# Kernel optimization log

Measured on AMD Instinct MI355X. Metric: run time of the kernel, lower is better.

The kernel has to match this reference:

```python
import jax, jax.numpy as jnp
import numpy as np

LATENT, COND, HID, OUT = 256, 64, 1024, 128
BATCH, MAX_LEN = 256, 512


def setup_inputs() -> dict:
    key = jax.random.key(0)
    ks = jax.random.split(key, 16)
    s = lambda fan_in: 1.0 / np.sqrt(fan_in)
    inp = {
        "latent_vector": jax.random.normal(ks[0], (BATCH, LATENT), jnp.float32),
        "conditions": jax.random.normal(ks[1], (BATCH, COND), jnp.float32),
        "output_lengths": jax.random.randint(ks[2], (BATCH,), 0, MAX_LEN, jnp.int32),
        # latent_to_hidden / latent_to_cell / latent_to_start
        "W_h": jax.random.uniform(ks[3], (HID, LATENT), jnp.float32, -s(LATENT), s(LATENT)),
        "b_h": jax.random.uniform(ks[4], (HID,), jnp.float32, -s(LATENT), s(LATENT)),
        "W_c": jax.random.uniform(ks[5], (HID, LATENT), jnp.float32, -s(LATENT), s(LATENT)),
        "b_c": jax.random.uniform(ks[6], (HID,), jnp.float32, -s(LATENT), s(LATENT)),
        "W_s": jax.random.uniform(ks[7], (OUT, LATENT), jnp.float32, -s(LATENT), s(LATENT)),
        "b_s": jax.random.uniform(ks[8], (OUT,), jnp.float32, -s(LATENT), s(LATENT)),
        # LSTM (PyTorch layout: gates i,f,g,o stacked -> 4*HID rows)
        "W_ih": jax.random.uniform(ks[9], (4 * HID, OUT + COND), jnp.float32, -s(HID), s(HID)),
        "W_hh": jax.random.uniform(ks[10], (4 * HID, HID), jnp.float32, -s(HID), s(HID)),
        "b_ih": jax.random.uniform(ks[11], (4 * HID,), jnp.float32, -s(HID), s(HID)),
        "b_hh": jax.random.uniform(ks[12], (4 * HID,), jnp.float32, -s(HID), s(HID)),
        # hidden_to_output
        "W_out": jax.random.uniform(ks[13], (OUT, HID), jnp.float32, -s(HID), s(HID)),
        "b_out": jax.random.uniform(ks[14], (OUT,), jnp.float32, -s(HID), s(HID)),
    }
    return inp


def reference(latent_vector, conditions, output_lengths, W_h, b_h, W_c, b_c, W_s, b_s,
              W_ih, W_hh, b_ih, b_hh, W_out, b_out):
    h0 = latent_vector @ W_h.T + b_h            # [B, HID]
    c0 = latent_vector @ W_c.T + b_c            # [B, HID]
    x0 = latent_vector @ W_s.T + b_s            # [B, OUT]
    bias = b_ih + b_hh                          # fuse the two LSTM biases

    def step(carry, _):
        h, c, x = carry
        inp = jnp.concatenate([x, conditions], axis=-1)   # [B, OUT+COND]
        gates = inp @ W_ih.T + h @ W_hh.T + bias          # [B, 4*HID]
        i, f, g, o = jnp.split(gates, 4, axis=-1)
        i = jax.nn.sigmoid(i)
        f = jax.nn.sigmoid(f)
        g = jnp.tanh(g)
        o = jax.nn.sigmoid(o)
        c_new = f * c + i * g
        h_new = o * jnp.tanh(c_new)
        y = h_new @ W_out.T + b_out                        # [B, OUT]
        return (h_new, c_new, y), y

    _, ys = jax.lax.scan(step, (h0, c0, x0), None, length=MAX_LEN)  # [T, B, OUT]
    outputs = jnp.transpose(ys, (1, 0, 2))                           # [B, T, OUT]
    # mask positions >= output_lengths[i] to zero
    t = jnp.arange(MAX_LEN)                                          # [T]
    mask = (t[None, :] < output_lengths[:, None]).astype(outputs.dtype)  # [B, T]
    return outputs * mask[:, :, None]
```

## Files before the change

kernel.cpp:

```cpp
#include <hip/hip_runtime.h>

#define BB   256
#define LAT  256
#define CND  64
#define HID  1024
#define OUTD 128
#define TLEN 512
#define GIN  192
#define G4   4096

typedef _Float16 f16x8 __attribute__((ext_vector_type(8)));
typedef float    f32x4 __attribute__((ext_vector_type(4)));

#define MFMA16(A,B,C) __builtin_amdgcn_mfma_f32_16x16x32_f16((A),(B),(C),0,0,0)

__device__ __forceinline__ float fsig(float x) {
  return 1.0f / (1.0f + exp2f(-1.4426950408889634f * x));
}
__device__ __forceinline__ float ftanh_(float x) {
  return 2.0f / (1.0f + exp2f(2.8853900817779268f * (-x))) - 1.0f;
}

__device__ __forceinline__ f16x8 ldg_sc_h8(const void* p) {
  f16x8 v;
  asm volatile("global_load_dwordx4 %0, %1, off sc0 sc1" : "=v"(v) : "v"(p));
  return v;
}
__device__ __forceinline__ void stg_sc_h(void* p, _Float16 v) {
  unsigned u = (unsigned)__builtin_bit_cast(unsigned short, v);
  asm volatile("global_store_short %0, %1, off sc0 sc1" :: "v"(p), "v"(u) : "memory");
}
__device__ __forceinline__ void stg_sc_f32(void* p, float v) {
  asm volatile("global_store_dword %0, %1, off sc0 sc1" :: "v"(p), "v"(v) : "memory");
}

template<int N> __device__ __forceinline__ void waitvm() {
  if constexpr (N == 8) asm volatile("s_waitcnt vmcnt(8)" ::: "memory");
  else                  asm volatile("s_waitcnt vmcnt(0)" ::: "memory");
  __builtin_amdgcn_sched_barrier(0);
}
#define LDSBAR() { asm volatile("s_waitcnt lgkmcnt(0)" ::: "memory"); \
                   __builtin_amdgcn_s_barrier(); \
                   __builtin_amdgcn_sched_barrier(0); }


__global__ void prep_init(const float* __restrict__ lat,
                          const float* __restrict__ Wh, const float* __restrict__ bh,
                          const float* __restrict__ Wc, const float* __restrict__ bc,
                          const float* __restrict__ Ws, const float* __restrict__ bs,
                          float* __restrict__ h0, _Float16* __restrict__ hF,
                          float* __restrict__ c0, float* __restrict__ x0)
{
  __shared__ float lat_s[8][LAT];
  int tid = threadIdx.x;
  int b0 = blockIdx.y * 8;
  for (int bb = 0; bb < 8; ++bb)
    lat_s[bb][tid] = lat[(size_t)(b0 + bb) * LAT + tid];
  __syncthreads();
  int col = blockIdx.x * 256 + tid;
  if (col >= 2 * HID + OUTD) return;
  const float* wr; float bias; int kind; int cc;
  if (col < HID)            { cc = col;           wr = Wh + (size_t)cc * LAT; bias = bh[cc]; kind = 0; }
  else if (col < 2 * HID)   { cc = col - HID;     wr = Wc + (size_t)cc * LAT; bias = bc[cc]; kind = 1; }
  else                      { cc = col - 2 * HID; wr = Ws + (size_t)cc * LAT; bias = bs[cc]; kind = 2; }
  float acc[8];
#pragma unroll
  for (int bb = 0; bb < 8; ++bb) acc[bb] = bias;
  for (int k = 0; k < LAT; ++k) {
    float wv = wr[k];
#pragma unroll
    for (int bb = 0; bb < 8; ++bb) acc[bb] += lat_s[bb][k] * wv;
  }
  for (int bb = 0; bb < 8; ++bb) {
    int b = b0 + bb;
    if (kind == 0) {
      float v = acc[bb];
      h0[(size_t)b*HID + cc] = v;
      hF[(size_t)b*HID + cc] = (_Float16)v;
    }
    else if (kind == 1) { c0[(size_t)b*HID + cc] = acc[bb]; }
    else                { x0[(size_t)b*OUTD + cc] = acc[bb]; }
  }
}

__global__ void prep_d(const float* __restrict__ h0, const float* __restrict__ Wout,
                       const float* __restrict__ bout, const float* __restrict__ x0,
                       float* __restrict__ d)
{
  int t = blockIdx.x * 256 + threadIdx.x;
  int b = t >> 7, o = t & 127;
  const float* wr = Wout + (size_t)o * HID;
  const float* hr = h0 + (size_t)b * HID;
  float acc = bout[o];
  for (int k = 0; k < HID; ++k) acc += hr[k] * wr[k];
  d[t] = x0[t] - acc;
}

__global__ void prep_weff(const float* __restrict__ Whh, const float* __restrict__ Wih,
                          const float* __restrict__ Wout, _Float16* __restrict__ WeffH)
{
  int k = blockIdx.x * 256 + threadIdx.x;
  int n0 = blockIdx.y * 16;
  float acc[16];
#pragma unroll
  for (int nn = 0; nn < 16; ++nn) acc[nn] = Whh[(size_t)(n0 + nn) * HID + k];
  for (int j = 0; j < OUTD; ++j) {
    float wo = Wout[(size_t)j * HID + k];
#pragma unroll
    for (int nn = 0; nn < 16; ++nn) acc[nn] += Wih[(size_t)(n0 + nn) * GIN + j] * wo;
  }
#pragma unroll
  for (int nn = 0; nn < 16; ++nn)
    WeffH[(size_t)(n0 + nn) * HID + k] = (_Float16)acc[nn];
}

__global__ void prep_wob(const float* __restrict__ Wout, _Float16* __restrict__ Wob) {
  int t = blockIdx.x * 256 + threadIdx.x;
  Wob[t] = (_Float16)Wout[t];
}

__global__ void prep_bias(const float* __restrict__ cond, const float* __restrict__ Wih,
                          const float* __restrict__ bih, const float* __restrict__ bhh,
                          const float* __restrict__ bout, const float* __restrict__ d,
                          float* __restrict__ biasR, float* __restrict__ biasS)
{
  __shared__ float cond_s[8][CND];
  __shared__ float d_s[8][OUTD];
  int tid = threadIdx.x;
  int b0 = blockIdx.y * 8;
  for (int qq = 0; qq < 2; ++qq) {
    int idx = qq * 256 + tid;
    cond_s[idx >> 6][idx & 63] = cond[(size_t)(b0 + (idx >> 6)) * CND + (idx & 63)];
  }
  for (int qq = 0; qq < 4; ++qq) {
    int idx = qq * 256 + tid;
    d_s[idx >> 7][idx & 127] = d[(size_t)(b0 + (idx >> 7)) * OUTD + (idx & 127)];
  }
  __syncthreads();
  int n = blockIdx.x * 256 + tid;
  const float* wi = Wih + (size_t)n * GIN;
  float base = bih[n] + bhh[n];
  float aR[8], aS[8];
#pragma unroll
  for (int bb = 0; bb < 8; ++bb) { aR[bb] = 0.f; aS[bb] = 0.f; }
  for (int c = 0; c < CND; ++c) {
    float wv = wi[OUTD + c];
#pragma unroll
    for (int bb = 0; bb < 8; ++bb) aR[bb] += cond_s[bb][c] * wv;
  }
  for (int o = 0; o < OUTD; ++o) {
    float wv = wi[o];
    float bo = bout[o];
#pragma unroll
    for (int bb = 0; bb < 8; ++bb) { aR[bb] += bo * wv; aS[bb] += d_s[bb][o] * wv; }
  }
  for (int bb = 0; bb < 8; ++bb) {
    size_t idx = (size_t)(b0 + bb) * G4 + n;
    biasR[idx] = base + aR[bb];
    biasS[idx] = base + aR[bb] + aS[bb];
  }
}


__global__ __launch_bounds__(256, 1)
void lstm_main(_Float16* hF, const float* __restrict__ c0g,
               const float* __restrict__ biasR, const float* __restrict__ biasS,
               const _Float16* __restrict__ WeffH, const _Float16* __restrict__ Wob,
               const float* __restrict__ bout, const int* __restrict__ len,
               float* __restrict__ out, unsigned* bar)
{
  __shared__ __align__(16) char lds[67584];
  const int wg = blockIdx.x;
  const int xcd = wg & 7, slot = wg >> 3;
  const int q = slot >> 2, mt = slot & 3;
  const int nt = q * 8 + xcd;
  const int tid = threadIdx.x;
  const int w = tid >> 6, lane = tid & 63;
  const int l15 = lane & 15, lh = lane >> 4;
  const int rowA = w * 16 + l15;
  const int bD0 = mt * 64 + w * 16 + lh * 4;
  const int j = nt * 16 + l15;
  const bool doy = (nt < 8);
  const int oy = doy ? nt * 16 + l15 : 0;
  const float bo = doy ? bout[oy] : 0.0f;

  const char* wb[4];
#pragma unroll
  for (int g = 0; g < 4; ++g)
    wb[g] = (const char*)(WeffH + ((size_t)(g * HID + nt * 16 + l15)) * HID + lh * 8);
  const char* wbY = (const char*)(Wob + (size_t)oy * HID + lh * 8);

  float c[4]; int mylen[4]; float biasRv[16];
#pragma unroll
  for (int r = 0; r < 4; ++r) {
    c[r] = c0g[(size_t)(bD0 + r) * HID + j];
    mylen[r] = len[bD0 + r];
    size_t bi = (size_t)(bD0 + r) * G4 + nt * 16 + l15;
#pragma unroll
    for (int g = 0; g < 4; ++g) biasRv[r * 4 + g] = biasR[bi + (size_t)g * HID];
  }

  const _Float16* cb0[8];
  int rc8[8];
#pragma unroll
  for (int i = 0; i < 8; ++i) {
    int s = i * 256 + tid;
    int r = s >> 5, cc = s & 31;
    cb0[i] = hF + ((size_t)(mt * 64 + r) * HID + cc * 8);
    rc8[i] = r * 528 + cc * 16;
  }
  const int rdoff = rowA * 528 + lh * 16;
  _Float16* hb0[4];
#pragma unroll
  for (int r = 0; r < 4; ++r) hb0[r] = hF + ((size_t)(bD0 + r) * HID + j);

  unsigned* const myarr = bar + (size_t)(mt * 8 + xcd) * 64;

  f32x4 accM[4], accyM;
  f16x8 pfb[2][8];

  for (int t = 0; t < TLEN; ++t) {
    const size_t parin  = (size_t)(t & 1) * (BB * HID);
    const size_t parout = (size_t)((t + 1) & 1) * (BB * HID);

    auto issue = [&](int K) {
#pragma unroll
      for (int i = 0; i < 8; ++i)
        pfb[K & 1][i] = ldg_sc_h8(cb0[i] + parin + K * 256);
    };
    auto dswr = [&](int K) {
      char* Bb = lds + (K & 1) * 33792;
#pragma unroll
      for (int i = 0; i < 8; ++i)
        *(f16x8*)(Bb + rc8[i]) = pfb[K & 1][i];
    };
    auto comp = [&](int K) {
      const char* Bb = lds + (K & 1) * 33792;
#pragma unroll
      for (int kc = 0; kc < 8; ++kc) {
        f16x8 aH = *(const f16x8*)(Bb + rdoff + kc * 64);
        const int wo = K * 512 + kc * 64;
#pragma unroll
        for (int g = 0; g < 4; ++g) {
          f16x8 wH = *(const f16x8*)(wb[g] + wo);
          accM[g] = MFMA16(aH, wH, accM[g]);
        }
        if (doy) {
          f16x8 wy = *(const f16x8*)(wbY + wo);
          accyM = MFMA16(aH, wy, accyM);
        }
      }
    };

    issue(0); issue(1);

#pragma unroll
    for (int r = 0; r < 4; ++r) {
#pragma unroll
      for (int g = 0; g < 4; ++g) accM[g][r] = biasRv[r * 4 + g];
      accyM[r] = bo;
    }
    if (t == 0) {
#pragma unroll
      for (int r = 0; r < 4; ++r) {
        size_t bi = (size_t)(bD0 + r) * G4 + nt * 16 + l15;
#pragma unroll
        for (int g = 0; g < 4; ++g) accM[g][r] = biasS[bi + (size_t)g * HID];
      }
    }

    waitvm<8>(); dswr(0); LDSBAR(); issue(2); comp(0);
    waitvm<8>(); dswr(1); LDSBAR(); issue(3); comp(1);
    waitvm<8>(); dswr(2); LDSBAR(); comp(2);
    waitvm<0>(); dswr(3); LDSBAR(); comp(3);

#pragma unroll
    for (int r = 0; r < 4; ++r) {
      float ig = fsig(accM[0][r]);
      float fg = fsig(accM[1][r]);
      float gg = ftanh_(accM[2][r]);
      float og = fsig(accM[3][r]);
      float cn = fg * c[r] + ig * gg;
      c[r] = cn;
      float hn = og * ftanh_(cn);
      stg_sc_h(hb0[r] + parout, (_Float16)hn);
    }
    if (doy && t > 0) {
      int tb = t - 1;
#pragma unroll
      for (int r = 0; r < 4; ++r) {
        float v = (tb < mylen[r]) ? accyM[r] : 0.0f;
        stg_sc_f32(out + ((size_t)(bD0 + r) * TLEN + tb) * OUTD + oy, v);
      }
    }

    asm volatile("s_waitcnt vmcnt(0)" ::: "memory");
    __syncthreads();
    if (tid < 64) {
      if (tid == 0)
        __hip_atomic_fetch_add(myarr, 1u, __ATOMIC_RELAXED, __HIP_MEMORY_SCOPE_AGENT);
      if (t < TLEN - 1 || doy) {
        unsigned tgt = 8u * (unsigned)(t + 1);
        long guard = 0;
        for (;;) {
          unsigned v = tgt;
          if (tid < 8)
            v = __hip_atomic_load(bar + (size_t)(mt * 8 + tid) * 64,
                                  __ATOMIC_RELAXED, __HIP_MEMORY_SCOPE_AGENT);
          if (__ballot(v >= tgt) == ~0ull) break;
          if (++guard > 2000000L) break;
          __builtin_amdgcn_s_sleep(2);
        }
      }
    }
    __syncthreads();
  }

  if (doy) {
    f32x4 aM;
#pragma unroll
    for (int r = 0; r < 4; ++r) aM[r] = bo;
    const _Float16* ebase = hF + (size_t)(mt * 64 + rowA) * HID + lh * 8;
    for (int b = 0; b < 8; ++b) {
      f16x8 e[4];
#pragma unroll
      for (int kc = 0; kc < 4; ++kc)
        e[kc] = ldg_sc_h8(ebase + b * 128 + kc * 32);
      asm volatile("s_waitcnt vmcnt(0)" ::: "memory");
      __builtin_amdgcn_sched_barrier(0);
#pragma unroll
      for (int kc = 0; kc < 4; ++kc) {
        f16x8 wy = *(const f16x8*)(wbY + b * 256 + kc * 64);
        aM = MFMA16(e[kc], wy, aM);
      }
    }
#pragma unroll
    for (int r = 0; r < 4; ++r) {
      float v = ((TLEN - 1) < mylen[r]) ? aM[r] : 0.0f;
      stg_sc_f32(out + ((size_t)(bD0 + r) * TLEN + (TLEN - 1)) * OUTD + oy, v);
    }
  }
}


extern "C" void kernel_launch(void* const* d_in, const int* in_sizes, int n_in,
                              void* d_out, int out_size, void* d_ws, size_t ws_size,
                              hipStream_t stream)
{
  const float* lat  = (const float*)d_in[0];
  const float* cond = (const float*)d_in[1];
  const int*   len  = (const int*)d_in[2];
  const float* Wh   = (const float*)d_in[3];
  const float* bh   = (const float*)d_in[4];
  const float* Wc   = (const float*)d_in[5];
  const float* bc   = (const float*)d_in[6];
  const float* Ws   = (const float*)d_in[7];
  const float* bs   = (const float*)d_in[8];
  const float* Wih  = (const float*)d_in[9];
  const float* Whh  = (const float*)d_in[10];
  const float* bih  = (const float*)d_in[11];
  const float* bhh  = (const float*)d_in[12];
  const float* Wout = (const float*)d_in[13];
  const float* bout = (const float*)d_in[14];
  float* out = (float*)d_out;

  char* ws = (char*)d_ws;
  size_t off = 0;
  auto alloc = [&](size_t bytes) -> void* {
    void* p = ws + off;
    off += (bytes + 255) & ~(size_t)255;
    return p;
  };
  _Float16* hF    = (_Float16*)alloc((size_t)2 * BB * HID * 2);
  float*    c0    = (float*)alloc((size_t)BB * HID * 4);
  float*    h0    = (float*)alloc((size_t)BB * HID * 4);
  float*    x0    = (float*)alloc((size_t)BB * OUTD * 4);
  float*    dxy   = (float*)alloc((size_t)BB * OUTD * 4);
  _Float16* Wob   = (_Float16*)alloc((size_t)OUTD * HID * 2);
  _Float16* WeffH = (_Float16*)alloc((size_t)G4 * HID * 2);
  float*    biasR = (float*)alloc((size_t)BB * G4 * 4);
  float*    biasS = (float*)alloc((size_t)BB * G4 * 4);
  unsigned* bar   = (unsigned*)alloc(4 * 8 * 64 * 4);
  if (off > ws_size) return;

  hipMemsetAsync(bar, 0, 4 * 8 * 64 * 4, stream);

  prep_init<<<dim3(9, 32),   256, 0, stream>>>(lat, Wh, bh, Wc, bc, Ws, bs, h0, hF, c0, x0);
  prep_weff<<<dim3(4, 256),  256, 0, stream>>>(Whh, Wih, Wout, WeffH);
  prep_wob <<<dim3(512),     256, 0, stream>>>(Wout, Wob);
  prep_d   <<<dim3(128),     256, 0, stream>>>(h0, Wout, bout, x0, dxy);
  prep_bias<<<dim3(16, 32),  256, 0, stream>>>(cond, Wih, bih, bhh, bout, dxy, biasR, biasS);
  lstm_main<<<dim3(256),     256, 0, stream>>>(hF, c0, biasR, biasS, WeffH, Wob, bout, len, out, bar);
}
```

Before: 11.35 ms.

## Issue all h-chunk loads upfront, swizzle LDS layout, signal barrier before output stores

All four K-chunks of the previous hidden state are now loaded up front into four register buffers and written into four separate LDS regions, so there is a single LDS barrier per step instead of four. The padded row stride is replaced by an XOR swizzle to avoid bank conflicts within a 512-byte row stride. The grid-barrier arrival is moved ahead of the masked output stores, which gives other blocks an earlier signal. The cost is double the LDS allocation (128KB) and more prefetch registers, which may affect register pressure and occupancy.

```diff
diff --git a/kernel.cpp b/kernel.cpp
--- a/kernel.cpp
+++ b/kernel.cpp
@@ -35,8 +35,10 @@
 }
 
 template<int N> __device__ __forceinline__ void waitvm() {
-  if constexpr (N == 8) asm volatile("s_waitcnt vmcnt(8)" ::: "memory");
-  else                  asm volatile("s_waitcnt vmcnt(0)" ::: "memory");
+  if constexpr (N == 24)      asm volatile("s_waitcnt vmcnt(24)" ::: "memory");
+  else if constexpr (N == 16) asm volatile("s_waitcnt vmcnt(16)" ::: "memory");
+  else if constexpr (N == 8)  asm volatile("s_waitcnt vmcnt(8)"  ::: "memory");
+  else                        asm volatile("s_waitcnt vmcnt(0)"  ::: "memory");
   __builtin_amdgcn_sched_barrier(0);
 }
 #define LDSBAR() { asm volatile("s_waitcnt lgkmcnt(0)" ::: "memory"); \
@@ -169,7 +171,7 @@
                const float* __restrict__ bout, const int* __restrict__ len,
                float* __restrict__ out, unsigned* bar)
 {
-  __shared__ __align__(16) char lds[67584];
+  __shared__ __align__(16) char lds[131072];
   const int wg = blockIdx.x;
   const int xcd = wg & 7, slot = wg >> 3;
   const int q = slot >> 2, mt = slot & 3;
@@ -207,9 +209,10 @@
     int s = i * 256 + tid;
     int r = s >> 5, cc = s & 31;
     cb0[i] = hF + ((size_t)(mt * 64 + r) * HID + cc * 8);
-    rc8[i] = r * 528 + cc * 16;
-  }
-  const int rdoff = rowA * 528 + lh * 16;
+    rc8[i] = r * 512 + ((cc * 16) ^ ((r & 7) << 4));
+  }
+  const int rdbase = rowA * 512;
+  const int rsw = (rowA & 7) << 4;
   _Float16* hb0[4];
 #pragma unroll
   for (int r = 0; r < 4; ++r) hb0[r] = hF + ((size_t)(bD0 + r) * HID + j);
@@ -217,7 +220,7 @@
   unsigned* const myarr = bar + (size_t)(mt * 8 + xcd) * 64;
 
   f32x4 accM[4], accyM;
-  f16x8 pfb[2][8];
+  f16x8 pfb[4][8];
 
   for (int t = 0; t < TLEN; ++t) {
     const size_t parin  = (size_t)(t & 1) * (BB * HID);
@@ -226,19 +229,19 @@
     auto issue = [&](int K) {
 #pragma unroll
       for (int i = 0; i < 8; ++i)
-        pfb[K & 1][i] = ldg_sc_h8(cb0[i] + parin + K * 256);
+        pfb[K][i] = ldg_sc_h8(cb0[i] + parin + K * 256);
     };
     auto dswr = [&](int K) {
-      char* Bb = lds + (K & 1) * 33792;
+      char* Bb = lds + K * 32768;
 #pragma unroll
       for (int i = 0; i < 8; ++i)
-        *(f16x8*)(Bb + rc8[i]) = pfb[K & 1][i];
+        *(f16x8*)(Bb + rc8[i]) = pfb[K][i];
     };
     auto comp = [&](int K) {
-      const char* Bb = lds + (K & 1) * 33792;
+      const char* Bb = lds + K * 32768;
 #pragma unroll
       for (int kc = 0; kc < 8; ++kc) {
-        f16x8 aH = *(const f16x8*)(Bb + rdoff + kc * 64);
+        f16x8 aH = *(const f16x8*)(Bb + rdbase + ((kc * 64 + lh * 16) ^ rsw));
         const int wo = K * 512 + kc * 64;
 #pragma unroll
         for (int g = 0; g < 4; ++g) {
@@ -252,7 +255,7 @@
       }
     };
 
-    issue(0); issue(1);
+    issue(0); issue(1); issue(2); issue(3);
 
 #pragma unroll
     for (int r = 0; r < 4; ++r) {
@@ -269,10 +272,12 @@
       }
     }
 
-    waitvm<8>(); dswr(0); LDSBAR(); issue(2); comp(0);
-    waitvm<8>(); dswr(1); LDSBAR(); issue(3); comp(1);
-    waitvm<8>(); dswr(2); LDSBAR(); comp(2);
-    waitvm<0>(); dswr(3); LDSBAR(); comp(3);
+    waitvm<24>(); dswr(0);
+    waitvm<16>(); dswr(1);
+    waitvm<8>();  dswr(2);
+    waitvm<0>();  dswr(3);
+    LDSBAR();
+    comp(0); comp(1); comp(2); comp(3);
 
 #pragma unroll
     for (int r = 0; r < 4; ++r) {
@@ -285,6 +290,11 @@
       float hn = og * ftanh_(cn);
       stg_sc_h(hb0[r] + parout, (_Float16)hn);
     }
+
+    asm volatile("s_waitcnt vmcnt(0)" ::: "memory");
+    __syncthreads();
+    if (tid == 0)
+      __hip_atomic_fetch_add(myarr, 1u, __ATOMIC_RELAXED, __HIP_MEMORY_SCOPE_AGENT);
     if (doy && t > 0) {
       int tb = t - 1;
 #pragma unroll
@@ -293,24 +303,17 @@
         stg_sc_f32(out + ((size_t)(bD0 + r) * TLEN + tb) * OUTD + oy, v);
       }
     }
-
-    asm volatile("s_waitcnt vmcnt(0)" ::: "memory");
-    __syncthreads();
-    if (tid < 64) {
-      if (tid == 0)
-        __hip_atomic_fetch_add(myarr, 1u, __ATOMIC_RELAXED, __HIP_MEMORY_SCOPE_AGENT);
-      if (t < TLEN - 1 || doy) {
-        unsigned tgt = 8u * (unsigned)(t + 1);
-        long guard = 0;
-        for (;;) {
-          unsigned v = tgt;
-          if (tid < 8)
-            v = __hip_atomic_load(bar + (size_t)(mt * 8 + tid) * 64,
-                                  __ATOMIC_RELAXED, __HIP_MEMORY_SCOPE_AGENT);
-          if (__ballot(v >= tgt) == ~0ull) break;
-          if (++guard > 2000000L) break;
-          __builtin_amdgcn_s_sleep(2);
-        }
+    if (tid < 64 && (t < TLEN - 1 || doy)) {
+      unsigned tgt = 8u * (unsigned)(t + 1);
+      long guard = 0;
+      for (;;) {
+        unsigned v = tgt;
+        if (tid < 8)
+          v = __hip_atomic_load(bar + (size_t)(mt * 8 + tid) * 64,
+                                __ATOMIC_RELAXED, __HIP_MEMORY_SCOPE_AGENT);
+        if (__ballot(v >= tgt) == ~0ull) break;
+        if (++guard > 2000000L) break;
+        __builtin_amdgcn_s_sleep(2);
       }
     }
     __syncthreads();
```

Measured after the change: 11.10 ms. 1.02x faster.
